# Kernel optimization log

Measured on AMD Instinct MI355X. Metric: run time of the kernel, lower is better.

Reference implementation:

```python
import jax, jax.numpy as jnp
import numpy as np

D_MODEL = 2048
NUM_HEADS = 16
D_HEAD = D_MODEL // NUM_HEADS
MAX_SEQ_LEN = 2048
THETA = 10000.0


def setup_inputs() -> dict:
    key = jax.random.key(0)
    kx, kq, kk, kv, ko = jax.random.split(key, 5)
    std = float(np.sqrt(2.0 / (D_MODEL + D_MODEL)))
    def tn(k):
        # truncated normal in [-3std, 3std] scaled by std
        return std * jax.random.truncated_normal(k, -3.0, 3.0, (D_MODEL, D_MODEL), jnp.float32)
    return {
        "x": jax.random.normal(kx, (2, MAX_SEQ_LEN, D_MODEL), jnp.float32),
        "w_q": tn(kq),
        "w_k": tn(kk),
        "w_v": tn(kv),
        "w_o": tn(ko),
    }


def _rope(x):
    # x: [B, H, S, Dh], default positions = arange(S)
    S = x.shape[-2]
    pos = jnp.arange(S, dtype=jnp.float32)
    inv_freq = 1.0 / (THETA ** (jnp.arange(0, D_HEAD, 2, dtype=jnp.float32) / D_HEAD))
    ang = pos[:, None] * inv_freq[None, :]           # [S, Dh/2]
    cos = jnp.cos(ang).astype(x.dtype)
    sin = jnp.sin(ang).astype(x.dtype)
    x_even = x[..., 0::2]
    x_odd = x[..., 1::2]
    out_even = x_even * cos - x_odd * sin
    out_odd = x_even * sin + x_odd * cos
    # interleave even/odd back
    return jnp.stack([out_even, out_odd], axis=-1).reshape(x.shape)


def reference(x, w_q, w_k, w_v, w_o):
    B, S, _ = x.shape
    def split_heads(t):
        return t.reshape(B, S, NUM_HEADS, D_HEAD).transpose(0, 2, 1, 3)  # [B,H,S,Dh]
    q = split_heads(x @ w_q.T)
    k = split_heads(x @ w_k.T)
    v = split_heads(x @ w_v.T)
    q = _rope(q)
    k = _rope(k)
    scores = jnp.einsum('bhqd,bhkd->bhqk', q, k) / jnp.sqrt(jnp.asarray(D_HEAD, x.dtype))
    causal = jnp.tril(jnp.ones((S, S), dtype=bool))
    scores = jnp.where(causal, scores, jnp.finfo(scores.dtype).min)
    attn = jax.nn.softmax(scores, axis=-1)
    out = jnp.einsum('bhqk,bhkd->bhqd', attn, v)     # [B,H,S,Dh]
    out = out.transpose(0, 2, 1, 3).reshape(B, S, D_MODEL)
    return out @ w_o.T
```

## Files before the change

### kernel.cpp

```cpp
#include <hip/hip_runtime.h>
#include <hip/hip_bf16.h>

typedef __bf16 bf16;
typedef __bf16 bf16x8 __attribute__((ext_vector_type(8)));
typedef __bf16 bf16x4 __attribute__((ext_vector_type(4)));
typedef float f32x4 __attribute__((ext_vector_type(4)));

#define MFMA_BF16(a, b, c) __builtin_amdgcn_mfma_f32_16x16x32_bf16(a, b, c, 0, 0, 0)

constexpr int D_MODEL = 2048;
constexpr int NUM_HEADS = 16;
constexpr int D_HEAD = 128;
constexpr int SEQ = 2048;
constexpr int BATCH = 2;
constexpr int M_TOTAL = BATCH * SEQ;

__device__ __forceinline__ void gld_lds16(const bf16* g, bf16* l) {
  __builtin_amdgcn_global_load_lds((const __attribute__((address_space(1))) void*)g,
                                   (__attribute__((address_space(3))) void*)l, 16, 0, 0);
}

__global__ __launch_bounds__(256) void cvt_all(const float* __restrict__ x,
                                               const float* __restrict__ wq,
                                               const float* __restrict__ wk,
                                               const float* __restrict__ wv,
                                               const float* __restrict__ wo,
                                               bf16* __restrict__ dst) {
  const long i = (long)blockIdx.x * 256 + threadIdx.x;
  const float* src;
  long off;
  if (i < 2097152) {
    src = x; off = i;
  } else {
    const long j = i - 2097152;
    const int w = (int)(j >> 20);
    off = j & 1048575;
    src = (w == 0) ? wq : (w == 1) ? wk : (w == 2) ? wv : wo;
  }
  float4 v = reinterpret_cast<const float4*>(src)[off];
  bf16x4 o;
  o[0] = (bf16)v.x; o[1] = (bf16)v.y; o[2] = (bf16)v.z; o[3] = (bf16)v.w;
  reinterpret_cast<bf16x4*>(dst)[i] = o;
}

enum { EP_F32 = 0, EP_QKV = 1 };

template <int EPI>
__global__ __launch_bounds__(512, 2) void gemm_bt(const bf16* __restrict__ A,
                                                  const bf16* __restrict__ B,
                                                  void* __restrict__ C0,
                                                  void* __restrict__ C1,
                                                  void* __restrict__ C2,
                                                  int M, int N, int K) {
  __shared__ __align__(16) bf16 As[3][256 * 64];
  __shared__ __align__(16) bf16 Bs[3][128 * 64];
  const int tid = threadIdx.x;
  const int lane = tid & 63;
  const int wave = tid >> 6;
  const int lane15 = lane & 15;
  const int quad = lane >> 4;

  const int nwg = gridDim.x;
  const int cpx = nwg >> 3;
  const int swz = (blockIdx.x & 7) * cpx + (blockIdx.x >> 3);
  const int NBX = N >> 7;
  const int m0 = (swz / NBX) * 256;
  const int n0 = (swz % NBX) * 128;

  const int wm = (wave >> 1) * 64;
  const int wn = (wave & 1) * 64;

  const int trow = tid >> 3;
  const int tchk = (tid & 7) ^ (trow & 7);
  const int wvoff = wave * 512;
  long a_off[4], b_off[2];
#pragma unroll
  for (int i = 0; i < 4; ++i) a_off[i] = (long)(m0 + i * 64 + trow) * K + tchk * 8;
#pragma unroll
  for (int i = 0; i < 2; ++i) b_off[i] = (long)(n0 + i * 64 + trow) * K + tchk * 8;

  const int r7 = lane15 & 7;
  const int ca0 = (quad ^ r7) * 8;
  const int ca1 = ((quad + 4) ^ r7) * 8;

  f32x4 acc[4][4];
#pragma unroll
  for (int i = 0; i < 4; ++i)
#pragma unroll
    for (int j = 0; j < 4; ++j) acc[i][j] = (f32x4){0.f, 0.f, 0.f, 0.f};

  const int NT = K >> 6;

#pragma unroll
  for (int i = 0; i < 4; ++i) gld_lds16(A + a_off[i], &As[0][i * 4096 + wvoff]);
#pragma unroll
  for (int i = 0; i < 2; ++i) gld_lds16(B + b_off[i], &Bs[0][i * 4096 + wvoff]);
#pragma unroll
  for (int i = 0; i < 4; ++i) gld_lds16(A + a_off[i] + 64, &As[1][i * 4096 + wvoff]);
#pragma unroll
  for (int i = 0; i < 2; ++i) gld_lds16(B + b_off[i] + 64, &Bs[1][i * 4096 + wvoff]);
  asm volatile("s_waitcnt vmcnt(6)" ::: "memory");
  __builtin_amdgcn_s_barrier();
  __builtin_amdgcn_sched_barrier(0);

  int bcur = 0, bstg = 2;
  for (int t = 0; t < NT; ++t) {
    const bf16* Ab = As[bcur];
    const bf16* Bb = Bs[bcur];
    const long kst = (long)(t + 2) * 64;
    const bool st = (t + 2 < NT);

    bf16x8 bfrg[4][2], afrg[2][2];
#pragma unroll
    for (int j = 0; j < 4; ++j) {
      const int rb = (wn + j * 16 + lane15) * 64;
      bfrg[j][0] = *reinterpret_cast<const bf16x8*>(&Bb[rb + ca0]);
      bfrg[j][1] = *reinterpret_cast<const bf16x8*>(&Bb[rb + ca1]);
    }
#pragma unroll
    for (int i = 0; i < 2; ++i) {
      const int ra = (wm + i * 16 + lane15) * 64;
      afrg[i][0] = *reinterpret_cast<const bf16x8*>(&Ab[ra + ca0]);
      afrg[i][1] = *reinterpret_cast<const bf16x8*>(&Ab[ra + ca1]);
    }
    if (st) {
#pragma unroll
      for (int i = 0; i < 3; ++i)
        gld_lds16(A + a_off[i] + kst, &As[bstg][i * 4096 + wvoff]);
    }
    __builtin_amdgcn_s_barrier();
    __builtin_amdgcn_sched_barrier(0);
    __builtin_amdgcn_s_setprio(1);
#pragma unroll
    for (int i = 0; i < 2; ++i)
#pragma unroll
      for (int j = 0; j < 4; ++j) {
        acc[i][j] = MFMA_BF16(afrg[i][0], bfrg[j][0], acc[i][j]);
        acc[i][j] = MFMA_BF16(afrg[i][1], bfrg[j][1], acc[i][j]);
      }
    __builtin_amdgcn_s_setprio(0);

#pragma unroll
    for (int i = 0; i < 2; ++i) {
      const int ra = (wm + (i + 2) * 16 + lane15) * 64;
      afrg[i][0] = *reinterpret_cast<const bf16x8*>(&Ab[ra + ca0]);
      afrg[i][1] = *reinterpret_cast<const bf16x8*>(&Ab[ra + ca1]);
    }
    if (st) {
      gld_lds16(A + a_off[3] + kst, &As[bstg][3 * 4096 + wvoff]);
      gld_lds16(B + b_off[0] + kst, &Bs[bstg][0 * 4096 + wvoff]);
      gld_lds16(B + b_off[1] + kst, &Bs[bstg][1 * 4096 + wvoff]);
    }
    __builtin_amdgcn_s_barrier();
    __builtin_amdgcn_sched_barrier(0);
    __builtin_amdgcn_s_setprio(1);
#pragma unroll
    for (int i = 0; i < 2; ++i)
#pragma unroll
      for (int j = 0; j < 4; ++j) {
        acc[i + 2][j] = MFMA_BF16(afrg[i][0], bfrg[j][0], acc[i + 2][j]);
        acc[i + 2][j] = MFMA_BF16(afrg[i][1], bfrg[j][1], acc[i + 2][j]);
      }
    __builtin_amdgcn_s_setprio(0);

    if (st) {
      asm volatile("s_waitcnt vmcnt(6)" ::: "memory");
      __builtin_amdgcn_s_barrier();
      __builtin_amdgcn_sched_barrier(0);
    } else if (t == NT - 2) {
      asm volatile("s_waitcnt vmcnt(0)" ::: "memory");
      __builtin_amdgcn_s_barrier();
      __builtin_amdgcn_sched_barrier(0);
    }
    bstg = bcur;
    bcur = (bcur == 2) ? 0 : bcur + 1;
  }

  if (EPI == EP_F32) {
#pragma unroll
    for (int i = 0; i < 4; ++i)
#pragma unroll
      for (int j = 0; j < 4; ++j)
#pragma unroll
        for (int r = 0; r < 4; ++r) {
          const int m = m0 + wm + i * 16 + quad * 4 + r;
          const int n = n0 + wn + j * 16 + lane15;
          reinterpret_cast<float*>(C0)[(long)m * N + n] = acc[i][j][r];
        }
  } else {
    const int mat = n0 >> 11;
    bf16* dst = (mat == 0) ? (bf16*)C0 : (mat == 1) ? (bf16*)C1 : (bf16*)C2;
    const int nb = n0 & 2047;
    if (mat < 2) {
#pragma unroll
      for (int i = 0; i < 4; ++i)
#pragma unroll
        for (int j = 0; j < 4; ++j)
#pragma unroll
          for (int r = 0; r < 4; ++r) {
            const int m = m0 + wm + i * 16 + quad * 4 + r;
            const int nl = nb + wn + j * 16 + lane15;
            const int b = m >> 11;
            const int s = m & (SEQ - 1);
            const int h = nl >> 7;
            const int d = nl & (D_HEAD - 1);
            float v = acc[i][j][r];
            float other = __shfl_xor(v, 1);
            float fr = exp2f((float)(d & ~1) * -0.103810253f);
            float ang = (float)s * fr;
            float sn = __sinf(ang);
            float cs = __cosf(ang);
            float outv = (lane15 & 1) ? (v * cs + other * sn) : (v * cs - other * sn);
            dst[(((long)(b * NUM_HEADS + h)) * SEQ + s) * D_HEAD + d] = (bf16)outv;
          }
    } else {
      const int h = nb >> 7;
#pragma unroll
      for (int i = 0; i < 4; ++i)
#pragma unroll
        for (int j = 0; j < 4; ++j) {
          bf16x4 pk;
#pragma unroll
          for (int r = 0; r < 4; ++r) pk[r] = (bf16)acc[i][j][r];
          const int m = m0 + wm + i * 16 + quad * 4;
          const int b = m >> 11;
          const int s = m & (SEQ - 1);
          const int d = wn + j * 16 + lane15;
          *reinterpret_cast<bf16x4*>(
              &dst[(((long)(b * NUM_HEADS + h)) * D_HEAD + d) * SEQ + s]) = pk;
        }
    }
  }
}

__global__ __launch_bounds__(256, 2) void flash_attn(const bf16* __restrict__ Q,
                                                     const bf16* __restrict__ K,
                                                     const bf16* __restrict__ Vt,
                                                     bf16* __restrict__ O) {
  __shared__ __align__(16) bf16 Kl[2][64 * 128];
  __shared__ __align__(16) bf16 Vl[2][128 * 64];
  __shared__ __align__(16) bf16 P[4 * 16 * 72];
  const int tid = threadIdx.x;
  const int lane = tid & 63;
  const int wave = tid >> 6;
  const int lane15 = lane & 15;
  const int quad = lane >> 4;
  const int idx = blockIdx.x >> 3;
  const int bh = (blockIdx.x & 7) * 4 + (idx & 3);
  const int qcg = 31 - (idx >> 2);
  const int qh = wave >> 1;
  const int ks = wave & 1;
  const int q0 = qcg * 64 + qh * 32;
  const long base = (long)bh * SEQ * D_HEAD;
  const bf16* qp = Q + base;
  const bf16* kp = K + base;
  const bf16* vp = Vt + base;
  bf16* Pw = &P[wave * 16 * 72];
  constexpr float scale = 0.08838834764831845f;
  constexpr float SMAX = 30.0f;

  int ksrc[4], vsrc[4];
  const int kdst = wave * 512;
#pragma unroll
  for (int i = 0; i < 4; ++i) {
    const int c = i * 256 + tid;
    const int krow = c >> 4;
    ksrc[i] = krow * D_HEAD + (((c & 15) ^ (krow & 15)) * 8);
    const int vd = c >> 3;
    vsrc[i] = vd * SEQ + (((c & 7) ^ (vd & 7)) * 8);
  }

  bf16x8 bq[2][4];
#pragma unroll
  for (int f = 0; f < 2; ++f)
#pragma unroll
    for (int kk = 0; kk < 4; ++kk)
      bq[f][kk] = *reinterpret_cast<const bf16x8*>(
          qp + (long)(q0 + f * 16 + lane15) * D_HEAD + kk * 32 + quad * 8);

  f32x4 o_acc[2][8];
#pragma unroll
  for (int f = 0; f < 2; ++f)
#pragma unroll
    for (int dj = 0; dj < 8; ++dj) o_acc[f][dj] = (f32x4){0.f, 0.f, 0.f, 0.f};
  float l_part[2] = {0.f, 0.f};

  const int nkt = qcg + 1;

#pragma unroll
  for (int i = 0; i < 4; ++i) gld_lds16(kp + ksrc[i], &Kl[0][i * 2048 + kdst]);
#pragma unroll
  for (int i = 0; i < 4; ++i) gld_lds16(vp + vsrc[i], &Vl[0][i * 2048 + kdst]);
  __syncthreads();

  for (int kt = 0; kt < nkt; ++kt) {
    const int k0 = kt * 64;
    const int buf = kt & 1;

    if (kt + 1 < nkt) {
      const int nk0 = k0 + 64;
#pragma unroll
      for (int i = 0; i < 4; ++i) gld_lds16(kp + nk0 * D_HEAD + ksrc[i], &Kl[buf ^ 1][i * 2048 + kdst]);
#pragma unroll
      for (int i = 0; i < 4; ++i) gld_lds16(vp + nk0 + vsrc[i], &Vl[buf ^ 1][i * 2048 + kdst]);
    }

    if ((kt & 1) == ks) {
      f32x4 sc[2][4];
#pragma unroll
      for (int f = 0; f < 2; ++f)
#pragma unroll
        for (int j = 0; j < 4; ++j) sc[f][j] = (f32x4){0.f, 0.f, 0.f, 0.f};
#pragma unroll
      for (int j = 0; j < 4; ++j) {
#pragma unroll
        for (int kk = 0; kk < 4; ++kk) {
          bf16x8 ak = *reinterpret_cast<const bf16x8*>(
              &Kl[buf][(j * 16 + lane15) * D_HEAD + (((kk * 4 + quad) ^ lane15) * 8)]);
          sc[0][j] = MFMA_BF16(ak, bq[0][kk], sc[0][j]);
          sc[1][j] = MFMA_BF16(ak, bq[1][kk], sc[1][j]);
        }
      }

      bf16x8 ap[2][2];
#pragma unroll
      for (int f = 0; f < 2; ++f) {
        const int qcol = q0 + f * 16 + lane15;
#pragma unroll
        for (int j = 0; j < 4; ++j) {
          bf16x4 pk;
#pragma unroll
          for (int r = 0; r < 4; ++r) {
            const int kpos = k0 + j * 16 + quad * 4 + r;
            float p = (kpos <= qcol) ? __expf(sc[f][j][r] * scale - SMAX) : 0.f;
            l_part[f] += p;
            pk[r] = (bf16)p;
          }
          *reinterpret_cast<bf16x4*>(&Pw[lane15 * 72 + j * 16 + quad * 4]) = pk;
        }
        ap[f][0] = *reinterpret_cast<const bf16x8*>(&Pw[lane15 * 72 + quad * 8]);
        ap[f][1] = *reinterpret_cast<const bf16x8*>(&Pw[lane15 * 72 + 32 + quad * 8]);
      }

#pragma unroll
      for (int kc = 0; kc < 2; ++kc) {
#pragma unroll
        for (int dj = 0; dj < 8; ++dj) {
          bf16x8 bv = *reinterpret_cast<const bf16x8*>(
              &Vl[buf][(dj * 16 + lane15) * 64 + (((kc * 4 + quad) ^ (lane15 & 7)) * 8)]);
          o_acc[0][dj] = MFMA_BF16(ap[0][kc], bv, o_acc[0][dj]);
          o_acc[1][dj] = MFMA_BF16(ap[1][kc], bv, o_acc[1][dj]);
        }
      }
    }

    __syncthreads();
  }

  __syncthreads();
  f32x4* dump = (f32x4*)&Kl[0][0];
  float* ldump = (float*)&Vl[0][0];
  if (ks == 1) {
#pragma unroll
    for (int f = 0; f < 2; ++f)
#pragma unroll
      for (int dj = 0; dj < 8; ++dj)
        dump[qh * 1024 + (f * 8 + dj) * 64 + lane] = o_acc[f][dj];
    ldump[qh * 128 + lane] = l_part[0];
    ldump[qh * 128 + 64 + lane] = l_part[1];
  }
  __syncthreads();
  if (ks == 0) {
#pragma unroll
    for (int f = 0; f < 2; ++f)
#pragma unroll
      for (int dj = 0; dj < 8; ++dj)
        o_acc[f][dj] = o_acc[f][dj] + dump[qh * 1024 + (f * 8 + dj) * 64 + lane];
    l_part[0] += ldump[qh * 128 + lane];
    l_part[1] += ldump[qh * 128 + 64 + lane];

    const int b = bh >> 4;
    const int h = bh & 15;
#pragma unroll
    for (int f = 0; f < 2; ++f) {
      float lsum = l_part[f];
      lsum += __shfl_xor(lsum, 16);
      lsum += __shfl_xor(lsum, 32);
#pragma unroll
      for (int r = 0; r < 4; ++r) {
        const float lr = __shfl(lsum, quad * 4 + r);
        const float inv_l = 1.0f / lr;
        const int qrow = q0 + f * 16 + quad * 4 + r;
#pragma unroll
        for (int dj = 0; dj < 8; ++dj)
          O[((long)b * SEQ + qrow) * D_MODEL + h * D_HEAD + dj * 16 + lane15] =
              (bf16)(o_acc[f][dj][r] * inv_l);
      }
    }
  }
}

extern "C" void kernel_launch(void* const* d_in, const int* in_sizes, int n_in,
                              void* d_out, int out_size, void* d_ws, size_t ws_size,
                              hipStream_t stream) {
  const float* x = (const float*)d_in[0];
  const float* wq = (const float*)d_in[1];
  const float* wk = (const float*)d_in[2];
  const float* wv = (const float*)d_in[3];
  const float* wo = (const float*)d_in[4];
  float* out = (float*)d_out;

  char* ws = (char*)d_ws;
  size_t off = 0;
  bf16* x_bf = (bf16*)(ws + off);  off += (size_t)M_TOTAL * D_MODEL * 2;
  bf16* wq_bf = (bf16*)(ws + off); off += (size_t)D_MODEL * D_MODEL * 2;
  bf16* wk_bf = (bf16*)(ws + off); off += (size_t)D_MODEL * D_MODEL * 2;
  bf16* wv_bf = (bf16*)(ws + off); off += (size_t)D_MODEL * D_MODEL * 2;
  bf16* wo_bf = (bf16*)(ws + off); off += (size_t)D_MODEL * D_MODEL * 2;
  bf16* q_r = (bf16*)(ws + off);   off += (size_t)M_TOTAL * D_MODEL * 2;
  bf16* k_r = (bf16*)(ws + off);   off += (size_t)M_TOTAL * D_MODEL * 2;
  bf16* vt_r = (bf16*)(ws + off);  off += (size_t)M_TOTAL * D_MODEL * 2;
  bf16* a_o = (bf16*)(ws + off);   off += (size_t)M_TOTAL * D_MODEL * 2;

  cvt_all<<<24576, dim3(256), 0, stream>>>(x, wq, wk, wv, wo, x_bf);

  gemm_bt<EP_QKV><<<dim3((M_TOTAL / 256) * (3 * D_MODEL / 128)), dim3(512), 0, stream>>>(
      x_bf, wq_bf, q_r, k_r, vt_r, M_TOTAL, 3 * D_MODEL, D_MODEL);

  flash_attn<<<dim3(1024), dim3(256), 0, stream>>>(q_r, k_r, vt_r, a_o);

  gemm_bt<EP_F32><<<dim3((M_TOTAL / 256) * (D_MODEL / 128)), dim3(512), 0, stream>>>(
      a_o, wo_bf, out, nullptr, nullptr, M_TOTAL, D_MODEL, D_MODEL);
}
```

Measured before the change: 361.7 us.

## Give each flash-attention wave its own query rows instead of splitting keys

Each block now covers 128 query rows, with each of the four waves owning 32 rows and walking every key tile up to its causal limit. Before, two waves shared 32 query rows and took alternate key tiles. This drops the LDS dump, the extra barrier and the cross-wave merge of partial accumulators, and halves the grid so each loaded K/V tile serves twice as many query rows. The cost is causal imbalance inside a block: waves with lower rows sit idle on the last tiles while still joining the per-tile barrier, and with only 512 blocks there may be less parallelism to spread across the GPU.

New measurement: 350.5 us. 1.03x faster.

```diff
diff --git a/kernel.cpp b/kernel.cpp
--- a/kernel.cpp
+++ b/kernel.cpp
@@ -247,10 +247,8 @@
   const int quad = lane >> 4;
   const int idx = blockIdx.x >> 3;
   const int bh = (blockIdx.x & 7) * 4 + (idx & 3);
-  const int qcg = 31 - (idx >> 2);
-  const int qh = wave >> 1;
-  const int ks = wave & 1;
-  const int q0 = qcg * 64 + qh * 32;
+  const int qg = 15 - (idx >> 2);
+  const int q0 = qg * 128 + wave * 32;
   const long base = (long)bh * SEQ * D_HEAD;
   const bf16* qp = Q + base;
   const bf16* kp = K + base;
@@ -285,7 +283,7 @@
     for (int dj = 0; dj < 8; ++dj) o_acc[f][dj] = (f32x4){0.f, 0.f, 0.f, 0.f};
   float l_part[2] = {0.f, 0.f};
 
-  const int nkt = qcg + 1;
+  const int nkt = 2 * qg + 2;
 
 #pragma unroll
   for (int i = 0; i < 4; ++i) gld_lds16(kp + ksrc[i], &Kl[0][i * 2048 + kdst]);
@@ -305,7 +303,7 @@
       for (int i = 0; i < 4; ++i) gld_lds16(vp + nk0 + vsrc[i], &Vl[buf ^ 1][i * 2048 + kdst]);
     }
 
-    if ((kt & 1) == ks) {
+    if (k0 <= q0 + 31) {
       f32x4 sc[2][4];
 #pragma unroll
       for (int f = 0; f < 2; ++f)
@@ -357,45 +355,22 @@
     __syncthreads();
   }
 
-  __syncthreads();
-  f32x4* dump = (f32x4*)&Kl[0][0];
-  float* ldump = (float*)&Vl[0][0];
-  if (ks == 1) {
-#pragma unroll
-    for (int f = 0; f < 2; ++f)
+  const int b = bh >> 4;
+  const int h = bh & 15;
+#pragma unroll
+  for (int f = 0; f < 2; ++f) {
+    float lsum = l_part[f];
+    lsum += __shfl_xor(lsum, 16);
+    lsum += __shfl_xor(lsum, 32);
+#pragma unroll
+    for (int r = 0; r < 4; ++r) {
+      const float lr = __shfl(lsum, quad * 4 + r);
+      const float inv_l = 1.0f / lr;
+      const int qrow = q0 + f * 16 + quad * 4 + r;
 #pragma unroll
       for (int dj = 0; dj < 8; ++dj)
-        dump[qh * 1024 + (f * 8 + dj) * 64 + lane] = o_acc[f][dj];
-    ldump[qh * 128 + lane] = l_part[0];
-    ldump[qh * 128 + 64 + lane] = l_part[1];
-  }
-  __syncthreads();
-  if (ks == 0) {
-#pragma unroll
-    for (int f = 0; f < 2; ++f)
-#pragma unroll
-      for (int dj = 0; dj < 8; ++dj)
-        o_acc[f][dj] = o_acc[f][dj] + dump[qh * 1024 + (f * 8 + dj) * 64 + lane];
-    l_part[0] += ldump[qh * 128 + lane];
-    l_part[1] += ldump[qh * 128 + 64 + lane];
-
-    const int b = bh >> 4;
-    const int h = bh & 15;
-#pragma unroll
-    for (int f = 0; f < 2; ++f) {
-      float lsum = l_part[f];
-      lsum += __shfl_xor(lsum, 16);
-      lsum += __shfl_xor(lsum, 32);
-#pragma unroll
-      for (int r = 0; r < 4; ++r) {
-        const float lr = __shfl(lsum, quad * 4 + r);
-        const float inv_l = 1.0f / lr;
-        const int qrow = q0 + f * 16 + quad * 4 + r;
-#pragma unroll
-        for (int dj = 0; dj < 8; ++dj)
-          O[((long)b * SEQ + qrow) * D_MODEL + h * D_HEAD + dj * 16 + lane15] =
-              (bf16)(o_acc[f][dj][r] * inv_l);
-      }
+        O[((long)b * SEQ + qrow) * D_MODEL + h * D_HEAD + dj * 16 + lane15] =
+            (bf16)(o_acc[f][dj][r] * inv_l);
     }
   }
 }
@@ -427,7 +402,7 @@
   gemm_bt<EP_QKV><<<dim3((M_TOTAL / 256) * (3 * D_MODEL / 128)), dim3(512), 0, stream>>>(
       x_bf, wq_bf, q_r, k_r, vt_r, M_TOTAL, 3 * D_MODEL, D_MODEL);
 
-  flash_attn<<<dim3(1024), dim3(256), 0, stream>>>(q_r, k_r, vt_r, a_o);
+  flash_attn<<<dim3(512), dim3(256), 0, stream>>>(q_r, k_r, vt_r, a_o);
 
   gemm_bt<EP_F32><<<dim3((M_TOTAL / 256) * (D_MODEL / 128)), dim3(512), 0, stream>>>(
       a_o, wo_bf, out, nullptr, nullptr, M_TOTAL, D_MODEL, D_MODEL);
```
